# Performance work log

Measured on AMD Instinct MI355X. Metric: run time of the kernel, lower is better.

## Reference

```python
import jax, jax.numpy as jnp
import numpy as np

IM_SIZE = (32, 32)
SIGMA = 5.0


def gaussian_2d_kernel(size, sigma):
    # Faithful port of the torch helper (meshgrid indexing='ij' over (W,H); square grid here).
    x_coords = jnp.arange(size[1], dtype=jnp.float32)
    y_coords = jnp.arange(size[0], dtype=jnp.float32)
    grid_x, grid_y = jnp.meshgrid(x_coords, y_coords, indexing='ij')
    center = (np.array(size, dtype=np.float32) - 1.0) / 2.0
    dist_sq = (grid_x - center[1]) ** 2 + (grid_y - center[0]) ** 2
    kernel_2d = jnp.exp(-0.5 * dist_sq / (sigma ** 2))
    return kernel_2d / kernel_2d.sum()


def setup_inputs() -> dict:
    rng = jax.random.key(0)
    k1, k2, k3 = jax.random.split(rng, 3)
    B, nH, T, H, W, C = 4, 4, 64, IM_SIZE[0], IM_SIZE[1], 8
    shape = (B, nH, T, H, W, C)
    return {
        'query': jax.random.normal(k1, shape, dtype=jnp.float32),
        'key': jax.random.normal(k2, shape, dtype=jnp.float32),
        'value': jax.random.normal(k3, shape, dtype=jnp.float32),
    }


def reference(query, key, value):
    B, nH, T, H, W, C = query.shape
    scale = jnp.float32(H * W)  # sqrt((H*W)^2)
    gauss_2d = gaussian_2d_kernel(IM_SIZE, SIGMA)  # [H, W] (square)
    # k_x: linear dot over flattened (H,W,C)
    q = query.reshape(B, nH, T, -1)
    k = key.reshape(B, nH, T, -1)
    dot_2d = jnp.einsum('bnpf,bnqf->bnpq', q, k) / scale  # [B,nH,T,T]
    # Original builds operator_val[b,n,p,q,h,w] = dot_2d[b,n,p,q]*gauss[h,w] then
    # contracts over q; the rank-1 Gaussian factors out of the q-contraction exactly:
    # out[b,n,p,m,d] = gauss_flat[m] * sum_q dot_2d[b,n,p,q] * val[b,n,q,m,d].
    val_2d = value.reshape(B, nH, T, H * W, -1)  # [B,nH,T,HW,d]
    out_2d = jnp.einsum('bnpq,bnqmd->bnpmd', dot_2d, val_2d)
    out_2d = out_2d * gauss_2d.reshape(1, 1, 1, H * W, 1)
    return out_2d.reshape(B, nH, T, H, W, -1)
```

## Files before the change

### kernel.cpp

```cpp
#include <hip/hip_runtime.h>
#include <cmath>

typedef __bf16 bf16x8 __attribute__((ext_vector_type(8)));
typedef float f32x4 __attribute__((ext_vector_type(4)));

#define HEADS 16
#define TT 64
#define FDIM 8192
#define NCHUNK 32
#define CHUNKF 256

__global__ __launch_bounds__(256) void qk_partial(const float* __restrict__ Q,
                                                  const float* __restrict__ Km,
                                                  __bf16* __restrict__ part) {
    const int chunk = blockIdx.x;
    const int h     = blockIdx.y;
    const int lane  = threadIdx.x & 63;
    const int w     = threadIdx.x >> 6;
    const int pr    = (w & 1) << 5;
    const int qr    = (w >> 1) << 5;
    const int r16   = lane & 15;
    const int g     = lane >> 4;
    const int kb    = chunk * CHUNKF + (g << 3);

    const float4* qp = (const float4*)(Q  + ((size_t)h * TT + pr + r16) * FDIM + kb);
    const float4* kp = (const float4*)(Km + ((size_t)h * TT + qr + r16) * FDIM + kb);

    f32x4 acc[2][2] = {{{0.f,0.f,0.f,0.f},{0.f,0.f,0.f,0.f}},
                       {{0.f,0.f,0.f,0.f},{0.f,0.f,0.f,0.f}}};

    #pragma unroll
    for (int ks = 0; ks < 8; ++ks) {
        bf16x8 a[2], b[2];
        #pragma unroll
        for (int t = 0; t < 2; ++t) {
            const float4 x0 = qp[(size_t)t * 32768 + ks * 8];
            const float4 x1 = qp[(size_t)t * 32768 + ks * 8 + 1];
            a[t][0]=(__bf16)x0.x; a[t][1]=(__bf16)x0.y; a[t][2]=(__bf16)x0.z; a[t][3]=(__bf16)x0.w;
            a[t][4]=(__bf16)x1.x; a[t][5]=(__bf16)x1.y; a[t][6]=(__bf16)x1.z; a[t][7]=(__bf16)x1.w;
            const float4 y0 = kp[(size_t)t * 32768 + ks * 8];
            const float4 y1 = kp[(size_t)t * 32768 + ks * 8 + 1];
            b[t][0]=(__bf16)y0.x; b[t][1]=(__bf16)y0.y; b[t][2]=(__bf16)y0.z; b[t][3]=(__bf16)y0.w;
            b[t][4]=(__bf16)y1.x; b[t][5]=(__bf16)y1.y; b[t][6]=(__bf16)y1.z; b[t][7]=(__bf16)y1.w;
        }
        #pragma unroll
        for (int i = 0; i < 2; ++i)
            #pragma unroll
            for (int j = 0; j < 2; ++j)
                acc[i][j] = __builtin_amdgcn_mfma_f32_16x16x32_bf16(a[i], b[j], acc[i][j], 0, 0, 0);
    }

    __bf16* pp = part + ((size_t)chunk * HEADS + h) * (TT * TT);
    #pragma unroll
    for (int i = 0; i < 2; ++i)
        #pragma unroll
        for (int j = 0; j < 2; ++j)
            #pragma unroll
            for (int r = 0; r < 4; ++r)
                pp[(pr + (i << 4) + (g << 2) + r) * TT + (qr + (j << 4) + r16)] =
                    (__bf16)acc[i][j][r];
}

__global__ __launch_bounds__(256) void reduce_sb(const unsigned int* __restrict__ partU,
                                                 __bf16* __restrict__ Sbf) {
    const int e = blockIdx.x * 256 + threadIdx.x;
    float s0 = 0.f, s1 = 0.f;
    #pragma unroll
    for (int c = 0; c < NCHUNK; ++c) {
        const unsigned int u = partU[(size_t)c * 32768 + e];
        s0 += __uint_as_float(u << 16);
        s1 += __uint_as_float(u & 0xffff0000u);
    }
    Sbf[2 * e]     = (__bf16)(s0 * (1.0f / 1024.0f));
    Sbf[2 * e + 1] = (__bf16)(s1 * (1.0f / 1024.0f));
}

__global__ __launch_bounds__(256) void sv_mfma(const float* __restrict__ V,
                                               const __bf16* __restrict__ Sbf,
                                               float* __restrict__ out,
                                               const float g_norm) {
    const int h    = blockIdx.y;
    const int lane = threadIdx.x & 63;
    const int w    = threadIdx.x >> 6;
    const int r16  = lane & 15;
    const int g    = lane >> 4;
    const int colbase = blockIdx.x * 128 + w * 32;

    const __bf16* Sh = Sbf + h * (TT * TT);
    bf16x8 a[4][2];
    #pragma unroll
    for (int pt = 0; pt < 4; ++pt)
        #pragma unroll
        for (int ks = 0; ks < 2; ++ks)
            a[pt][ks] = *(const bf16x8*)(Sh + (pt * 16 + r16) * TT + ks * 32 + g * 8);

    const float* Vh = V + (size_t)h * TT * FDIM;
    f32x4 acc[4][2] = {};

    #pragma unroll
    for (int jt = 0; jt < 2; ++jt) {
        #pragma unroll
        for (int ks = 0; ks < 2; ++ks) {
            float vf[8];
            #pragma unroll
            for (int i = 0; i < 8; ++i)
                vf[i] = Vh[(size_t)(ks * 32 + g * 8 + i) * FDIM + colbase + jt * 16 + r16];
            bf16x8 b;
            #pragma unroll
            for (int i = 0; i < 8; ++i) b[i] = (__bf16)vf[i];
            #pragma unroll
            for (int pt = 0; pt < 4; ++pt)
                acc[pt][jt] = __builtin_amdgcn_mfma_f32_16x16x32_bf16(a[pt][ks], b, acc[pt][jt], 0, 0, 0);
        }
    }

    #pragma unroll
    for (int jt = 0; jt < 2; ++jt) {
        const int col = colbase + jt * 16 + r16;
        const int m   = col >> 3;
        const float dx = (float)(m >> 5) - 15.5f;
        const float dy = (float)(m & 31) - 15.5f;
        const float gg = expf(-(dx * dx + dy * dy) * 0.02f) * g_norm;
        #pragma unroll
        for (int pt = 0; pt < 4; ++pt)
            #pragma unroll
            for (int r = 0; r < 4; ++r) {
                const int p = pt * 16 + (g << 2) + r;
                __builtin_nontemporal_store(acc[pt][jt][r] * gg,
                    &out[(size_t)h * TT * FDIM + (size_t)p * FDIM + col]);
            }
    }
}

extern "C" void kernel_launch(void* const* d_in, const int* in_sizes, int n_in,
                              void* d_out, int out_size, void* d_ws, size_t ws_size,
                              hipStream_t stream) {
    const float* Q  = (const float*)d_in[0];
    const float* Km = (const float*)d_in[1];
    const float* V  = (const float*)d_in[2];
    float* out = (float*)d_out;
    __bf16* Sbf  = (__bf16*)d_ws;
    __bf16* part = (__bf16*)d_out;

    double sx = 0.0;
    for (int x = 0; x < 32; ++x) { const double d = (double)x - 15.5; sx += exp(-d * d / 50.0); }
    const float g_norm = (float)(1.0 / (sx * sx));

    qk_partial<<<dim3(NCHUNK, HEADS), 256, 0, stream>>>(Q, Km, part);
    reduce_sb<<<dim3(128), 256, 0, stream>>>((const unsigned int*)part, Sbf);
    sv_mfma<<<dim3(FDIM / 128, HEADS), 256, 0, stream>>>(V, Sbf, out, g_norm);
}
```

Before: 37.55 us.

## Fuse split-K partial reduction into SV kernel and halve QK chunk count

The separate reduce kernel is removed. Each SV block now sums the bf16 QK partials for its head directly into shared memory, and the 1/1024 scale is folded into the Gaussian factor. NCHUNK is halved (16 chunks of 512 features) so there are fewer partials to reduce, at the cost of fewer QK blocks and less parallelism in the first kernel. Partials go in the workspace when it is large enough, which removes one launch, though every SV block re-reads the head's partials redundantly.

```diff
diff --git a/kernel.cpp b/kernel.cpp
--- a/kernel.cpp
+++ b/kernel.cpp
@@ -7,8 +7,9 @@
 #define HEADS 16
 #define TT 64
 #define FDIM 8192
-#define NCHUNK 32
-#define CHUNKF 256
+#define NCHUNK 16
+#define CHUNKF 512
+#define PART_BYTES ((size_t)NCHUNK * HEADS * TT * TT * 2)
 
 __global__ __launch_bounds__(256) void qk_partial(const float* __restrict__ Q,
                                                   const float* __restrict__ Km,
@@ -30,7 +31,7 @@
                        {{0.f,0.f,0.f,0.f},{0.f,0.f,0.f,0.f}}};
 
     #pragma unroll
-    for (int ks = 0; ks < 8; ++ks) {
+    for (int ks = 0; ks < CHUNKF / 32; ++ks) {
         bf16x8 a[2], b[2];
         #pragma unroll
         for (int t = 0; t < 2; ++t) {
@@ -59,6 +60,91 @@
             for (int r = 0; r < 4; ++r)
                 pp[(pr + (i << 4) + (g << 2) + r) * TT + (qr + (j << 4) + r16)] =
                     (__bf16)acc[i][j][r];
+}
+
+__global__ __launch_bounds__(256) void sv_fused(const float* __restrict__ V,
+                                                const __bf16* __restrict__ part,
+                                                float* __restrict__ out,
+                                                const float g_scale) {
+    __shared__ __bf16 Slds[TT * 72];
+
+    const int h    = blockIdx.y;
+    const int tid  = threadIdx.x;
+    const int lane = tid & 63;
+    const int w    = tid >> 6;
+    const int r16  = lane & 15;
+    const int g    = lane >> 4;
+    const int colbase = blockIdx.x * 128 + w * 32;
+
+    {
+        const unsigned int* pu = (const unsigned int*)part;
+        float s[16];
+        #pragma unroll
+        for (int i = 0; i < 16; ++i) s[i] = 0.f;
+        #pragma unroll
+        for (int c = 0; c < NCHUNK; ++c) {
+            const unsigned int* b = pu + ((size_t)c * HEADS + h) * 2048 + tid * 8;
+            const uint4 u0 = *(const uint4*)(b);
+            const uint4 u1 = *(const uint4*)(b + 4);
+            const unsigned int uu[8] = {u0.x, u0.y, u0.z, u0.w, u1.x, u1.y, u1.z, u1.w};
+            #pragma unroll
+            for (int i = 0; i < 8; ++i) {
+                s[2 * i]     += __uint_as_float(uu[i] << 16);
+                s[2 * i + 1] += __uint_as_float(uu[i] & 0xffff0000u);
+            }
+        }
+        bf16x8 h0, h1;
+        #pragma unroll
+        for (int i = 0; i < 8; ++i) { h0[i] = (__bf16)s[i]; h1[i] = (__bf16)s[i + 8]; }
+        __bf16* dst = Slds + (tid >> 2) * 72 + (tid & 3) * 16;
+        *(bf16x8*)(dst)     = h0;
+        *(bf16x8*)(dst + 8) = h1;
+    }
+    __syncthreads();
+
+    bf16x8 a[4][2];
+    #pragma unroll
+    for (int pt = 0; pt < 4; ++pt)
+        #pragma unroll
+        for (int ks = 0; ks < 2; ++ks)
+            a[pt][ks] = *(const bf16x8*)(Slds + (pt * 16 + r16) * 72 + ks * 32 + g * 8);
+
+    const float* Vh = V + (size_t)h * TT * FDIM;
+    f32x4 acc[4][2] = {};
+
+    #pragma unroll
+    for (int jt = 0; jt < 2; ++jt) {
+        #pragma unroll
+        for (int ks = 0; ks < 2; ++ks) {
+            float vf[8];
+            #pragma unroll
+            for (int i = 0; i < 8; ++i)
+                vf[i] = Vh[(size_t)(ks * 32 + g * 8 + i) * FDIM + colbase + jt * 16 + r16];
+            bf16x8 b;
+            #pragma unroll
+            for (int i = 0; i < 8; ++i) b[i] = (__bf16)vf[i];
+            #pragma unroll
+            for (int pt = 0; pt < 4; ++pt)
+                acc[pt][jt] = __builtin_amdgcn_mfma_f32_16x16x32_bf16(a[pt][ks], b, acc[pt][jt], 0, 0, 0);
+        }
+    }
+
+    #pragma unroll
+    for (int jt = 0; jt < 2; ++jt) {
+        const int col = colbase + jt * 16 + r16;
+        const int m   = col >> 3;
+        const float dx = (float)(m >> 5) - 15.5f;
+        const float dy = (float)(m & 31) - 15.5f;
+        const float gg = expf(-(dx * dx + dy * dy) * 0.02f) * g_scale;
+        #pragma unroll
+        for (int pt = 0; pt < 4; ++pt)
+            #pragma unroll
+            for (int r = 0; r < 4; ++r) {
+                const int p = pt * 16 + (g << 2) + r;
+                __builtin_nontemporal_store(acc[pt][jt][r] * gg,
+                    &out[(size_t)h * TT * FDIM + (size_t)p * FDIM + col]);
+            }
+    }
 }
 
 __global__ __launch_bounds__(256) void reduce_sb(const unsigned int* __restrict__ partU,
@@ -139,14 +225,21 @@
     const float* Km = (const float*)d_in[1];
     const float* V  = (const float*)d_in[2];
     float* out = (float*)d_out;
-    __bf16* Sbf  = (__bf16*)d_ws;
-    __bf16* part = (__bf16*)d_out;
 
     double sx = 0.0;
     for (int x = 0; x < 32; ++x) { const double d = (double)x - 15.5; sx += exp(-d * d / 50.0); }
-    const float g_norm = (float)(1.0 / (sx * sx));
-
-    qk_partial<<<dim3(NCHUNK, HEADS), 256, 0, stream>>>(Q, Km, part);
-    reduce_sb<<<dim3(128), 256, 0, stream>>>((const unsigned int*)part, Sbf);
-    sv_mfma<<<dim3(FDIM / 128, HEADS), 256, 0, stream>>>(V, Sbf, out, g_norm);
-}
+    const float g_norm  = (float)(1.0 / (sx * sx));
+    const float g_scale = g_norm * (1.0f / 1024.0f);
+
+    if (ws_size >= PART_BYTES) {
+        __bf16* part = (__bf16*)d_ws;
+        qk_partial<<<dim3(NCHUNK, HEADS), 256, 0, stream>>>(Q, Km, part);
+        sv_fused<<<dim3(FDIM / 128, HEADS), 256, 0, stream>>>(V, part, out, g_scale);
+    } else {
+        __bf16* part = (__bf16*)d_out;
+        __bf16* Sbf  = (__bf16*)d_ws;
+        qk_partial<<<dim3(NCHUNK, HEADS), 256, 0, stream>>>(Q, Km, part);
+        reduce_sb<<<dim3(128), 256, 0, stream>>>((const unsigned int*)part, Sbf);
+        sv_mfma<<<dim3(FDIM / 128, HEADS), 256, 0, stream>>>(V, Sbf, out, g_norm);
+    }
+}
```

Result: slower. 38.39 us (+2.2%).
